# Kernel tuning notes

Measured on AMD Instinct MI355X. Metric: run time of the kernel, lower is better.

## Reference

```python
import jax, jax.numpy as jnp
from jax import lax
import numpy as np

N, C, H, W = 8, 32, 64, 64
KS, NB = 7, 6            # kernel_size, num_bases
TB = (KS // 2) * NB      # total_bases = 18
BC = TB * NB             # bc_dim = 108
INTER = max(64, BC // 2) # 64
OUT = 64
PAD = KS // 2
EPS = 1e-5


def conv3x3(x, w, b):
    # x: (N,Cin,H,W), w: (Cout,Cin,3,3)
    y = lax.conv_general_dilated(x, w, (1, 1), [(1, 1), (1, 1)],
                                 dimension_numbers=('NCHW', 'OIHW', 'NCHW'))
    return y + b[None, :, None, None]


def batchnorm(x, g, b):
    # training-mode BN: batch stats over (N,H,W)
    mu = jnp.mean(x, axis=(0, 2, 3), keepdims=True)
    var = jnp.var(x, axis=(0, 2, 3), keepdims=True)
    return (x - mu) * lax.rsqrt(var + EPS) * g[None, :, None, None] + b[None, :, None, None]


def setup_inputs() -> dict:
    key = jax.random.key(0)
    ks = jax.random.split(key, 12)
    s = 0.05
    # random bases as in get_random_bases: (TB, KS*KS), zero-mean-ish rows
    f = jax.random.normal(ks[0], (TB, KS * KS), dtype=jnp.float32)
    bases = f - jnp.mean(f, axis=1, keepdims=True) / jnp.std(f, axis=1, keepdims=True)
    return {
        'x': jax.random.normal(ks[1], (N, C, H, W), dtype=jnp.float32),
        'conv1_w': jax.random.normal(ks[2], (INTER, C, 3, 3), dtype=jnp.float32) * s,
        'conv1_b': jax.random.normal(ks[3], (INTER,), dtype=jnp.float32) * s,
        'bn1_g': jnp.ones((INTER,), jnp.float32),
        'bn1_b': jnp.zeros((INTER,), jnp.float32),
        'conv2_w': jax.random.normal(ks[4], (BC, INTER, 3, 3), dtype=jnp.float32) * s,
        'conv2_b': jax.random.normal(ks[5], (BC,), dtype=jnp.float32) * s,
        'bn2_g': jnp.ones((BC,), jnp.float32),
        'bn2_b': jnp.zeros((BC,), jnp.float32),
        'bases': bases,
        'out_w': jax.random.normal(ks[6], (OUT, C * NB), dtype=jnp.float32) * s,
        'out_b': jax.random.normal(ks[7], (OUT,), dtype=jnp.float32) * s,
    }


def reference(x, conv1_w, conv1_b, bn1_g, bn1_b, conv2_w, conv2_b,
              bn2_g, bn2_b, bases, out_w, out_b):
    # bases_net: conv3x3 -> BN -> tanh -> conv3x3 -> BN -> tanh
    h = jnp.tanh(batchnorm(conv3x3(x, conv1_w, conv1_b), bn1_g, bn1_b))
    coef = jnp.tanh(batchnorm(conv3x3(h, conv2_w, conv2_b), bn2_g, bn2_b))
    # (N, BC, H, W) -> (N, NB, TB, H, W) -> (N, H, W, NB, TB)
    coef = coef.reshape(N, NB, TB, H, W).transpose(0, 3, 4, 1, 2)
    # atoms: (coef[...,None] * bases).sum(-2).transpose(-1,-2) => (N,H,W,KS^2,NB)
    atoms = jnp.einsum('nhwmt,tk->nhwkm', coef, bases)
    # unfold: channel-major (C, ks, ks) flattened, matching F.unfold
    patches = lax.conv_general_dilated_patches(
        x, (KS, KS), (1, 1), [(PAD, PAD), (PAD, PAD)],
        dimension_numbers=('NCHW', 'OIHW', 'NCHW'))  # (N, C*KS*KS, H, W)
    patches = patches.reshape(N, C, KS * KS, H, W)
    # per-pixel contraction over ks^2: (N,H,W,C,NB)
    bases_out = jnp.einsum('nckhw,nhwkm->nhwcm', patches, atoms)
    bases_out = bases_out.reshape(N, H, W, C * NB)
    out = jnp.einsum('nhwd,od->nohw', bases_out, out_w) + out_b[None, :, None, None]
    return out
```

## Files before the change

### kernel.cpp

```cpp
#include <hip/hip_runtime.h>
#include <hip/hip_bf16.h>

#define N_ 8
#define C_ 32
#define H_ 64
#define W_ 64
#define HW_ (H_*W_)
#define NHW_ (N_*HW_)
#define INTER_ 64
#define BC_ 108
#define KS_ 7
#define K2_ (KS_*KS_)
#define NB_ 6
#define TB_ 18
#define OUT_ 64
#define DDIM_ (C_*NB_)
#define P2CH_ 288

typedef __attribute__((ext_vector_type(8))) short short8;
typedef __attribute__((ext_vector_type(4))) float f32x4;
typedef __attribute__((ext_vector_type(2))) float f32x2;

__device__ __forceinline__ unsigned short f2bf(float f) {
    union { float f; unsigned u; } v; v.f = f;
    unsigned r = v.u + 0x7fffu + ((v.u >> 16) & 1u);
    return (unsigned short)(r >> 16);
}
__device__ __forceinline__ float bf2f(unsigned short h) {
    return __uint_as_float((unsigned int)h << 16);
}

__device__ __forceinline__ short8 frag4(const unsigned int* p) {
    union { unsigned int u[4]; short8 s; } v;
    v.u[0] = p[0]; v.u[1] = p[1]; v.u[2] = p[2]; v.u[3] = p[3];
    return v.s;
}

__inline__ __device__ float wave_reduce_sum(float v) {
    #pragma unroll
    for (int off = 32; off > 0; off >>= 1) v += __shfl_down(v, off);
    return v;
}

template<int TP0, int NTP>
__device__ __forceinline__ void pconv_pass(const float (*sx)[44],
                                           const float* __restrict__ bases,
                                           unsigned int* __restrict__ P2,
                                           int n, int c, int r0, int rb, int lane) {
    f32x2 av[NTP][4];
    #pragma unroll
    for (int tp = 0; tp < NTP; tp++)
        #pragma unroll
        for (int rr = 0; rr < 4; rr++) av[tp][rr] = (f32x2){0.f, 0.f};

    #pragma unroll 1
    for (int kx = 0; kx < 7; kx++) {
        float rw[12];
        const float* sp = &sx[lane + kx][rb];
        #pragma unroll
        for (int qq = 0; qq < 3; qq++) {
            float4 r4 = *(const float4*)(sp + qq * 4);
            rw[qq * 4 + 0] = r4.x; rw[qq * 4 + 1] = r4.y;
            rw[qq * 4 + 2] = r4.z; rw[qq * 4 + 3] = r4.w;
        }
        #pragma unroll
        for (int tp = 0; tp < NTP; tp++) {
            #pragma unroll
            for (int ky = 0; ky < 7; ky++) {
                f32x2 w2;
                w2.x = bases[(2 * (TP0 + tp)) * K2_ + ky * 7 + kx];
                w2.y = bases[(2 * (TP0 + tp) + 1) * K2_ + ky * 7 + kx];
                #pragma unroll
                for (int rr = 0; rr < 4; rr++) {
                    float xv = rw[rr + ky];
                    f32x2 xv2 = (f32x2){xv, xv};
                    av[tp][rr] += xv2 * w2;
                }
            }
        }
    }

    #pragma unroll
    for (int tp = 0; tp < NTP; tp++)
        #pragma unroll
        for (int rr = 0; rr < 4; rr++) {
            int gr = r0 + rb + rr;
            unsigned int pk = (unsigned int)f2bf(av[tp][rr].x) |
                              ((unsigned int)f2bf(av[tp][rr].y) << 16);
            P2[(((size_t)n * P2CH_ + (TP0 + tp) * 32 + c) << 12) + (gr << 6) + lane] = pk;
        }
}

__global__ __launch_bounds__(256) void k_front(const float* __restrict__ x,
                                               const float* __restrict__ bases,
                                               const float* __restrict__ w1,
                                               const float* __restrict__ w2,
                                               const float* __restrict__ ow,
                                               unsigned short* __restrict__ xb,
                                               unsigned short* __restrict__ wb1,
                                               unsigned short* __restrict__ wb2,
                                               unsigned short* __restrict__ wbp,
                                               unsigned int* __restrict__ P2) {
    __shared__ __align__(16) char smem[70 * 44 * 4];
    int bid = blockIdx.x, t = threadIdx.x;

    if (bid < 1024) {
        float (*sx)[44] = (float(*)[44])smem;
        int rq = bid & 3;
        int c  = (bid >> 2) & 31;
        int n  = bid >> 7;
        int lane = t & 63, wv = t >> 6;
        int r0 = rq << 4;

        const float* xc = x + (((size_t)n * C_ + c) << 12);
        #pragma unroll
        for (int j = 0; j < 6; j++) {
            int p = wv + 4 * j;
            if (p < 22) {
                int grow = r0 - 3 + p;
                bool rowok = (grow >= 0 && grow < H_);
                int wx = lane - 3;
                float v = 0.f;
                if (rowok && wx >= 0) v = xc[(grow << 6) + wx];
                sx[lane][p] = v;
                if (lane < 6) {
                    int wx2 = 61 + lane;
                    float v2 = 0.f;
                    if (rowok && wx2 < W_) v2 = xc[(grow << 6) + wx2];
                    sx[64 + lane][p] = v2;
                }
            }
        }
        __syncthreads();

        int rb = wv * 4;
        pconv_pass<0, 5>(sx, bases, P2, n, c, r0, rb, lane);
        pconv_pass<5, 4>(sx, bases, P2, n, c, r0, rb, lane);
    } else {
        int pbid = bid - 1024;
        if (pbid < 512) {
            unsigned short* sT = (unsigned short*)smem;
            int n = pbid >> 6, hw0 = (pbid << 6) & 4095;
            for (int i = t; i < 2048; i += 256) {
                int c = i >> 6, px = i & 63;
                float v = x[(((size_t)n * C_ + c) << 12) + hw0 + px];
                sT[px * 36 + c] = f2bf(v);
            }
            __syncthreads();
            unsigned int* xd = (unsigned int*)xb;
            for (int i = t; i < 1024; i += 256) {
                int px = i >> 4, cw = i & 15;
                unsigned int lo = sT[px * 36 + cw * 2], hi = sT[px * 36 + cw * 2 + 1];
                xd[(((size_t)n << 12) + hw0 + px) * 16 + cw] = lo | (hi << 16);
            }
        } else if (pbid < 584) {
            int i = (pbid - 512) * 256 + t;
            int ci = i & 31, co = (i >> 5) & 63, s = i >> 11;
            wb1[i] = f2bf(w1[((co << 5) + ci) * 9 + s]);
        } else if (pbid < 872) {
            int i = (pbid - 584) * 256 + t;
            int ci = i & 63, co = (i >> 6) & 127, s = i >> 13;
            unsigned short v = 0;
            if (co < BC_) v = f2bf(w2[((co << 6) + ci) * 9 + s]);
            wb2[i] = v;
        } else {
            int i = (pbid - 872) * 256 + t;
            if (i < OUT_ * DDIM_) {
                float v = ow[i];
                unsigned short hi = f2bf(v);
                wbp[i] = hi;
                wbp[OUT_ * DDIM_ + i] = f2bf(v - bf2f(hi));
            }
        }
    }
}

template<int CIN, int COG, int ROWS, int WPAD, int NCOQ>
__global__ __launch_bounds__(256) void k_conv3(const unsigned short* __restrict__ xb,
                                               const unsigned short* __restrict__ wb,
                                               const float* __restrict__ bias,
                                               float* __restrict__ y,
                                               int COUT_real) {
    constexpr int CPAD = CIN + 8;
    constexpr int NSLC = (ROWS + 2) * 66;
    constexpr int MT = COG / 16;
    constexpr int NTW = ROWS;
    constexpr int KSTEPS = CIN / 32;
    __shared__ unsigned short sx[NSLC * CPAD];
    __shared__ unsigned short sw[9 * COG * CPAD];

    int bid = blockIdx.x;
    int coq = bid % NCOQ;
    int rp = (bid / NCOQ) % (H_ / ROWS);
    int n = bid / (NCOQ * (H_ / ROWS));
    int h0 = rp * ROWS;
    int co0 = coq * COG;
    int t = threadIdx.x;
    int lane = t & 63, wv = t >> 6;
    int q = lane >> 4, n15 = lane & 15;

    {
        const unsigned int* xg = (const unsigned int*)xb + (size_t)n * HW_ * (CIN / 2);
        unsigned int* sxd = (unsigned int*)sx;
        constexpr int DW = CIN / 2;
        constexpr int DWPT = DW / 8;
        int part = t & 7;
        for (int sl = (t >> 3); sl < NSLC; sl += 32) {
            int r = sl / 66, col = sl % 66;
            int hh = h0 - 1 + r, ww = col - 1;
            unsigned int v[DWPT];
            #pragma unroll
            for (int i = 0; i < DWPT; i++) v[i] = 0;
            if (hh >= 0 && hh < H_ && ww >= 0 && ww < W_) {
                const unsigned int* gp = xg + (size_t)(hh * W_ + ww) * DW + part * DWPT;
                #pragma unroll
                for (int i = 0; i < DWPT; i++) v[i] = gp[i];
            }
            unsigned int* d = sxd + sl * (CPAD / 2) + part * DWPT;
            #pragma unroll
            for (int i = 0; i < DWPT; i++) d[i] = v[i];
        }
    }
    {
        const unsigned int* wg = (const unsigned int*)wb;
        unsigned int* swd = (unsigned int*)sw;
        constexpr int TOT = 9 * COG * (CIN / 2);
        for (int e = t; e < TOT; e += 256) {
            int s_co = e / (CIN / 2), cw = e % (CIN / 2);
            int s = s_co / COG, co = s_co % COG;
            swd[s_co * (CPAD / 2) + cw] = wg[((size_t)s * WPAD + co0 + co) * (CIN / 2) + cw];
        }
    }
    __syncthreads();

    f32x4 acc[NTW][MT];
    #pragma unroll
    for (int a = 0; a < NTW; a++)
        #pragma unroll
        for (int m = 0; m < MT; m++) acc[a][m] = (f32x4){0.f, 0.f, 0.f, 0.f};

    #pragma unroll
    for (int s = 0; s < 9; s++) {
        int dy = s / 3, dx = s % 3;
        #pragma unroll
        for (int kc = 0; kc < KSTEPS; kc++) {
            int ci0 = kc * 32;
            short8 bfr[NTW];
            #pragma unroll
            for (int ntl = 0; ntl < NTW; ntl++) {
                int nt = wv * NTW + ntl;
                int r_out = nt >> 2, col0 = (nt & 3) * 16;
                bfr[ntl] = *(const short8*)(sx + ((r_out + dy) * 66 + col0 + n15 + dx) * CPAD + ci0 + q * 8);
            }
            #pragma unroll
            for (int mt = 0; mt < MT; mt++) {
                short8 afr = *(const short8*)(sw + ((s * COG) + mt * 16 + n15) * CPAD + ci0 + q * 8);
                #pragma unroll
                for (int ntl = 0; ntl < NTW; ntl++)
                    acc[ntl][mt] = __builtin_amdgcn_mfma_f32_16x16x32_bf16(afr, bfr[ntl], acc[ntl][mt], 0, 0, 0);
            }
        }
    }

    #pragma unroll
    for (int ntl = 0; ntl < NTW; ntl++) {
        int nt = wv * NTW + ntl;
        int h = h0 + (nt >> 2), wcol = (nt & 3) * 16 + n15;
        #pragma unroll
        for (int mt = 0; mt < MT; mt++) {
            #pragma unroll
            for (int reg = 0; reg < 4; reg++) {
                int co = co0 + mt * 16 + q * 4 + reg;
                if (co < COUT_real)
                    y[(((size_t)n * COUT_real + co) << 12) + h * W_ + wcol] = acc[ntl][mt][reg] + bias[co];
            }
        }
    }
}

__global__ __launch_bounds__(256) void k_bnpart(const float* __restrict__ y,
                                                float2* __restrict__ part, int Cout) {
    int bid = blockIdx.x;
    int c = bid >> 3, n = bid & 7;
    int t = threadIdx.x;
    const float* p = y + (((size_t)n * Cout + c) << 12) + t * 16;
    float s = 0.f, s2 = 0.f;
    #pragma unroll
    for (int j = 0; j < 4; j++) {
        float4 v = *(const float4*)(p + j * 4);
        s += v.x + v.y + v.z + v.w;
        s2 += v.x * v.x + v.y * v.y + v.z * v.z + v.w * v.w;
    }
    s = wave_reduce_sum(s);
    s2 = wave_reduce_sum(s2);
    __shared__ float sm[8];
    int wid = t >> 6, lane = t & 63;
    if (lane == 0) { sm[wid] = s; sm[4 + wid] = s2; }
    __syncthreads();
    if (t == 0) {
        float2 r;
        r.x = sm[0] + sm[1] + sm[2] + sm[3];
        r.y = sm[4] + sm[5] + sm[6] + sm[7];
        part[c * 8 + n] = r;
    }
}

__global__ __launch_bounds__(256) void k_bntr(const float* __restrict__ y1,
                                              const float2* __restrict__ part,
                                              const float* __restrict__ g,
                                              const float* __restrict__ bb,
                                              unsigned short* __restrict__ y1b) {
    __shared__ unsigned short sT[64 * 68];
    __shared__ float scs[INTER_], shs[INTER_];
    int bid = blockIdx.x, t = threadIdx.x;
    int n = bid >> 6, hw0 = (bid << 6) & 4095;
    if (t < INTER_) {
        float s = 0.f, s2 = 0.f;
        #pragma unroll
        for (int j = 0; j < 8; j++) { float2 p = part[t * 8 + j]; s += p.x; s2 += p.y; }
        float mu = s / (float)NHW_, var = s2 / (float)NHW_ - mu * mu;
        float sc = g[t] * rsqrtf(var + 1e-5f);
        scs[t] = sc; shs[t] = bb[t] - mu * sc;
    }
    __syncthreads();
    for (int i = t; i < 4096; i += 256) {
        int c = i >> 6, px = i & 63;
        float v = y1[(((size_t)n * INTER_ + c) << 12) + hw0 + px];
        sT[px * 68 + c] = f2bf(tanhf(v * scs[c] + shs[c]));
    }
    __syncthreads();
    unsigned int* yd = (unsigned int*)y1b;
    for (int i = t; i < 2048; i += 256) {
        int px = i >> 5, cw = i & 31;
        unsigned int lo = sT[px * 68 + cw * 2], hi = sT[px * 68 + cw * 2 + 1];
        yd[(((size_t)n << 12) + hw0 + px) * 32 + cw] = lo | (hi << 16);
    }
}

#define YPAD_ 97
__global__ __launch_bounds__(256) void k_ytail(const float* __restrict__ y2,
                                               const float2* __restrict__ part,
                                               const float* __restrict__ g,
                                               const float* __restrict__ bb,
                                               const unsigned int* __restrict__ P2,
                                               const unsigned short* __restrict__ wbp,
                                               const float* __restrict__ out_b,
                                               float* __restrict__ out) {
    __shared__ float scs[BC_], shs[BC_];
    __shared__ float cfs[BC_][32];
    __shared__ unsigned int sYh[32 * YPAD_];
    __shared__ unsigned int sYl[32 * YPAD_];

    int bid = blockIdx.x;
    int n = bid >> 7, px0 = (bid & 127) << 5;
    int t = threadIdx.x;

    int px = t & 31, cg = t >> 5;
    unsigned int u[4][9];
    {
        const unsigned int* Pb = P2 + (((size_t)n * P2CH_) << 12) + px0 + px;
        #pragma unroll
        for (int cc = 0; cc < 4; cc++) {
            int c = cg * 4 + cc;
            #pragma unroll
            for (int tp = 0; tp < 9; tp++)
                u[cc][tp] = Pb[(size_t)(tp * 32 + c) << 12];
        }
    }

    if (t < BC_) {
        float s = 0.f, s2 = 0.f;
        #pragma unroll
        for (int j = 0; j < 8; j++) { float2 p = part[t * 8 + j]; s += p.x; s2 += p.y; }
        float mu = s / (float)NHW_, var = s2 / (float)NHW_ - mu * mu;
        float sc = g[t] * rsqrtf(var + 1e-5f);
        scs[t] = sc; shs[t] = bb[t] - mu * sc;
    }
    __syncthreads();

    for (int i = t; i < BC_ * 32; i += 256) {
        int ch = i >> 5, pxx = i & 31;
        float v = y2[(((size_t)n * BC_ + ch) << 12) + px0 + pxx];
        cfs[ch][pxx] = tanhf(v * scs[ch] + shs[ch]);
    }
    __syncthreads();

    {
        f32x2 pv2[2][TB_];
        #pragma unroll
        for (int j = 0; j < 2; j++)
            #pragma unroll
            for (int tp = 0; tp < 9; tp++) {
                pv2[j][2 * tp].x     = __uint_as_float(u[2 * j][tp] << 16);
                pv2[j][2 * tp].y     = __uint_as_float(u[2 * j + 1][tp] << 16);
                pv2[j][2 * tp + 1].x = __uint_as_float(u[2 * j][tp] & 0xffff0000u);
                pv2[j][2 * tp + 1].y = __uint_as_float(u[2 * j + 1][tp] & 0xffff0000u);
            }
        f32x2 ym2[2][NB_];
        #pragma unroll
        for (int j = 0; j < 2; j++)
            #pragma unroll
            for (int m = 0; m < NB_; m++) ym2[j][m] = (f32x2){0.f, 0.f};
        #pragma unroll
        for (int m = 0; m < NB_; m++)
            #pragma unroll
            for (int tt = 0; tt < TB_; tt++) {
                float cfv = cfs[m * TB_ + tt][px];
                f32x2 c2 = (f32x2){cfv, cfv};
                ym2[0][m] += c2 * pv2[0][tt];
                ym2[1][m] += c2 * pv2[1][tt];
            }
        #pragma unroll
        for (int j = 0; j < 2; j++) {
            #pragma unroll
            for (int half = 0; half < 2; half++) {
                int c = cg * 4 + 2 * j + half;
                #pragma unroll
                for (int jj = 0; jj < 3; jj++) {
                    float y0 = half ? ym2[j][2 * jj].y     : ym2[j][2 * jj].x;
                    float y1v = half ? ym2[j][2 * jj + 1].y : ym2[j][2 * jj + 1].x;
                    unsigned short h0 = f2bf(y0);
                    unsigned short h1 = f2bf(y1v);
                    unsigned short l0 = f2bf(y0 - bf2f(h0));
                    unsigned short l1 = f2bf(y1v - bf2f(h1));
                    sYh[px * YPAD_ + c * 3 + jj] = (unsigned int)h0 | ((unsigned int)h1 << 16);
                    sYl[px * YPAD_ + c * 3 + jj] = (unsigned int)l0 | ((unsigned int)l1 << 16);
                }
            }
        }
    }
    __syncthreads();

    int lane = t & 63, wv = t >> 6;
    int q = lane >> 4, n15 = lane & 15;
    f32x4 acc[2];
    acc[0] = (f32x4){0.f, 0.f, 0.f, 0.f};
    acc[1] = (f32x4){0.f, 0.f, 0.f, 0.f};
    #pragma unroll
    for (int ks = 0; ks < 6; ks++) {
        short8 ah = *(const short8*)(wbp + (wv * 16 + n15) * DDIM_ + ks * 32 + q * 8);
        short8 al = *(const short8*)(wbp + OUT_ * DDIM_ + (wv * 16 + n15) * DDIM_ + ks * 32 + q * 8);
        #pragma unroll
        for (int nt = 0; nt < 2; nt++) {
            short8 bh = frag4(sYh + (nt * 16 + n15) * YPAD_ + ks * 16 + q * 4);
            short8 bl = frag4(sYl + (nt * 16 + n15) * YPAD_ + ks * 16 + q * 4);
            acc[nt] = __builtin_amdgcn_mfma_f32_16x16x32_bf16(ah, bh, acc[nt], 0, 0, 0);
            acc[nt] = __builtin_amdgcn_mfma_f32_16x16x32_bf16(ah, bl, acc[nt], 0, 0, 0);
            acc[nt] = __builtin_amdgcn_mfma_f32_16x16x32_bf16(al, bh, acc[nt], 0, 0, 0);
        }
    }
    #pragma unroll
    for (int nt = 0; nt < 2; nt++)
        #pragma unroll
        for (int reg = 0; reg < 4; reg++) {
            int o = wv * 16 + q * 4 + reg;
            out[(((size_t)n * OUT_ + o) << 12) + px0 + nt * 16 + n15] = acc[nt][reg] + out_b[o];
        }
}

extern "C" void kernel_launch(void* const* d_in, const int* in_sizes, int n_in,
                              void* d_out, int out_size, void* d_ws, size_t ws_size,
                              hipStream_t stream) {
    const float* x       = (const float*)d_in[0];
    const float* conv1_w = (const float*)d_in[1];
    const float* conv1_b = (const float*)d_in[2];
    const float* bn1_g   = (const float*)d_in[3];
    const float* bn1_b   = (const float*)d_in[4];
    const float* conv2_w = (const float*)d_in[5];
    const float* conv2_b = (const float*)d_in[6];
    const float* bn2_g   = (const float*)d_in[7];
    const float* bn2_b   = (const float*)d_in[8];
    const float* bases   = (const float*)d_in[9];
    const float* out_w   = (const float*)d_in[10];
    const float* out_b   = (const float*)d_in[11];
    float* out = (float*)d_out;

    float* y1  = (float*)d_ws;
    float* y2  = y1 + (size_t)N_ * INTER_ * HW_;
    unsigned int* P2 = (unsigned int*)(y2 + (size_t)N_ * BC_ * HW_);
    unsigned short* xb  = (unsigned short*)(P2 + (size_t)N_ * P2CH_ * HW_);
    unsigned short* y1b = xb + (size_t)NHW_ * C_;
    unsigned short* wb1 = y1b + (size_t)NHW_ * INTER_;
    unsigned short* wb2 = wb1 + 9 * 64 * 32;
    unsigned short* wbp = wb2 + 9 * 128 * 64;
    float2* part1 = (float2*)(wbp + 2 * OUT_ * DDIM_);
    float2* part2 = part1 + INTER_ * 8;

    k_front<<<1944, 256, 0, stream>>>(x, bases, conv1_w, conv2_w, out_w,
                                      xb, wb1, wb2, wbp, P2);

    k_conv3<C_, 64, 1, 64, 1><<<N_ * 64, 256, 0, stream>>>(
        xb, wb1, conv1_b, y1, INTER_);
    k_bnpart<<<INTER_ * 8, 256, 0, stream>>>(y1, part1, INTER_);
    k_bntr<<<512, 256, 0, stream>>>(y1, part1, bn1_g, bn1_b, y1b);

    k_conv3<INTER_, 16, 2, 128, 7><<<N_ * 32 * 7, 256, 0, stream>>>(
        y1b, wb2, conv2_b, y2, BC_);
    k_bnpart<<<BC_ * 8, 256, 0, stream>>>(y2, part2, BC_);

    k_ytail<<<1024, 256, 0, stream>>>(y2, (const float2*)part2, bn2_g, bn2_b,
                                      P2, wbp, out_b, out);
}
```

Before: 178.2 us.

## Fuse fp32-to-bf16 conversion into conv1 and merge BN1 stats into front kernel

Conv1 now reads fp32 x and fp32 weights directly, converting to bf16 while staging into shared memory. This removes the separate x transpose/convert pass and the weight prepack. The pixel-conv pass, BN1 partial statistics, and conv2/out weight packing are merged into one mid kernel launched after conv1, which drops one launch. In exchange, conv1 does strided per-channel global reads and every block repeats the weight conversion.

New measurement: 178.4 us. About the same (+0.1%).

```diff
diff --git a/kernel.cpp b/kernel.cpp
--- a/kernel.cpp
+++ b/kernel.cpp
@@ -91,16 +91,92 @@
         }
 }
 
-__global__ __launch_bounds__(256) void k_front(const float* __restrict__ x,
-                                               const float* __restrict__ bases,
-                                               const float* __restrict__ w1,
-                                               const float* __restrict__ w2,
-                                               const float* __restrict__ ow,
-                                               unsigned short* __restrict__ xb,
-                                               unsigned short* __restrict__ wb1,
-                                               unsigned short* __restrict__ wb2,
-                                               unsigned short* __restrict__ wbp,
-                                               unsigned int* __restrict__ P2) {
+__global__ __launch_bounds__(256) void k_conv1raw(const float* __restrict__ x,
+                                                  const float* __restrict__ w1,
+                                                  const float* __restrict__ bias,
+                                                  float* __restrict__ y) {
+    constexpr int CPAD = 40;
+    constexpr int NSLC = 3 * 66;
+    __shared__ unsigned short sx[NSLC * CPAD];
+    __shared__ unsigned short sw[9 * 64 * CPAD];
+
+    int bid = blockIdx.x;
+    int h0 = bid & 63;
+    int n = bid >> 6;
+    int t = threadIdx.x;
+    int lane = t & 63, wv = t >> 6;
+    int q = lane >> 4, n15 = lane & 15;
+
+    {
+        int part = t & 7;
+        for (int sl = (t >> 3); sl < NSLC; sl += 32) {
+            int r = sl / 66, col = sl % 66;
+            int hh = h0 - 1 + r, ww = col - 1;
+            unsigned int d0 = 0, d1 = 0;
+            if (hh >= 0 && hh < H_ && ww >= 0 && ww < W_) {
+                const float* xp = x + ((size_t)n * C_ + part * 4) * HW_ + hh * W_ + ww;
+                unsigned short b0 = f2bf(xp[0]);
+                unsigned short b1 = f2bf(xp[HW_]);
+                unsigned short b2 = f2bf(xp[2 * HW_]);
+                unsigned short b3 = f2bf(xp[3 * HW_]);
+                d0 = (unsigned int)b0 | ((unsigned int)b1 << 16);
+                d1 = (unsigned int)b2 | ((unsigned int)b3 << 16);
+            }
+            unsigned int* d = (unsigned int*)sx + sl * (CPAD / 2) + part * 2;
+            d[0] = d0; d[1] = d1;
+        }
+    }
+    {
+        #pragma unroll 2
+        for (int f = t * 8; f < t * 8 + 8; f++) {
+            int co = f >> 5, ci = f & 31;
+            const float* wp = w1 + (size_t)f * 9;
+            #pragma unroll
+            for (int s = 0; s < 9; s++)
+                sw[(s * 64 + co) * CPAD + ci] = f2bf(wp[s]);
+        }
+    }
+    __syncthreads();
+
+    f32x4 acc[4];
+    #pragma unroll
+    for (int m = 0; m < 4; m++) acc[m] = (f32x4){0.f, 0.f, 0.f, 0.f};
+
+    #pragma unroll
+    for (int s = 0; s < 9; s++) {
+        int dy = s / 3, dx = s % 3;
+        int nt = wv;
+        int col0 = (nt & 3) * 16;
+        short8 bfr = *(const short8*)(sx + (dy * 66 + col0 + n15 + dx) * CPAD + q * 8);
+        #pragma unroll
+        for (int mt = 0; mt < 4; mt++) {
+            short8 afr = *(const short8*)(sw + ((s * 64) + mt * 16 + n15) * CPAD + q * 8);
+            acc[mt] = __builtin_amdgcn_mfma_f32_16x16x32_bf16(afr, bfr, acc[mt], 0, 0, 0);
+        }
+    }
+
+    {
+        int wcol = (wv & 3) * 16 + n15;
+        #pragma unroll
+        for (int mt = 0; mt < 4; mt++) {
+            #pragma unroll
+            for (int reg = 0; reg < 4; reg++) {
+                int co = mt * 16 + q * 4 + reg;
+                y[(((size_t)n * INTER_ + co) << 12) + h0 * W_ + wcol] = acc[mt][reg] + bias[co];
+            }
+        }
+    }
+}
+
+__global__ __launch_bounds__(256) void k_mid(const float* __restrict__ x,
+                                             const float* __restrict__ bases,
+                                             const float* __restrict__ y1,
+                                             const float* __restrict__ w2,
+                                             const float* __restrict__ ow,
+                                             unsigned int* __restrict__ P2,
+                                             float2* __restrict__ part1,
+                                             unsigned short* __restrict__ wb2,
+                                             unsigned short* __restrict__ wbp) {
     __shared__ __align__(16) char smem[70 * 44 * 4];
     int bid = blockIdx.x, t = threadIdx.x;
 
@@ -136,64 +212,61 @@
         int rb = wv * 4;
         pconv_pass<0, 5>(sx, bases, P2, n, c, r0, rb, lane);
         pconv_pass<5, 4>(sx, bases, P2, n, c, r0, rb, lane);
+    } else if (bid < 1536) {
+        int pb = bid - 1024;
+        int c = pb >> 3, n = pb & 7;
+        const float* p = y1 + (((size_t)n * INTER_ + c) << 12) + t * 16;
+        float s = 0.f, s2 = 0.f;
+        #pragma unroll
+        for (int j = 0; j < 4; j++) {
+            float4 v = *(const float4*)(p + j * 4);
+            s += v.x + v.y + v.z + v.w;
+            s2 += v.x * v.x + v.y * v.y + v.z * v.z + v.w * v.w;
+        }
+        s = wave_reduce_sum(s);
+        s2 = wave_reduce_sum(s2);
+        float* sm = (float*)smem;
+        int wid = t >> 6, lane = t & 63;
+        if (lane == 0) { sm[wid] = s; sm[4 + wid] = s2; }
+        __syncthreads();
+        if (t == 0) {
+            float2 r;
+            r.x = sm[0] + sm[1] + sm[2] + sm[3];
+            r.y = sm[4] + sm[5] + sm[6] + sm[7];
+            part1[c * 8 + n] = r;
+        }
+    } else if (bid < 1824) {
+        int i = (bid - 1536) * 256 + t;
+        int ci = i & 63, co = (i >> 6) & 127, s = i >> 13;
+        unsigned short v = 0;
+        if (co < BC_) v = f2bf(w2[((co << 6) + ci) * 9 + s]);
+        wb2[i] = v;
     } else {
-        int pbid = bid - 1024;
-        if (pbid < 512) {
-            unsigned short* sT = (unsigned short*)smem;
-            int n = pbid >> 6, hw0 = (pbid << 6) & 4095;
-            for (int i = t; i < 2048; i += 256) {
-                int c = i >> 6, px = i & 63;
-                float v = x[(((size_t)n * C_ + c) << 12) + hw0 + px];
-                sT[px * 36 + c] = f2bf(v);
-            }
-            __syncthreads();
-            unsigned int* xd = (unsigned int*)xb;
-            for (int i = t; i < 1024; i += 256) {
-                int px = i >> 4, cw = i & 15;
-                unsigned int lo = sT[px * 36 + cw * 2], hi = sT[px * 36 + cw * 2 + 1];
-                xd[(((size_t)n << 12) + hw0 + px) * 16 + cw] = lo | (hi << 16);
-            }
-        } else if (pbid < 584) {
-            int i = (pbid - 512) * 256 + t;
-            int ci = i & 31, co = (i >> 5) & 63, s = i >> 11;
-            wb1[i] = f2bf(w1[((co << 5) + ci) * 9 + s]);
-        } else if (pbid < 872) {
-            int i = (pbid - 584) * 256 + t;
-            int ci = i & 63, co = (i >> 6) & 127, s = i >> 13;
-            unsigned short v = 0;
-            if (co < BC_) v = f2bf(w2[((co << 6) + ci) * 9 + s]);
-            wb2[i] = v;
-        } else {
-            int i = (pbid - 872) * 256 + t;
-            if (i < OUT_ * DDIM_) {
-                float v = ow[i];
-                unsigned short hi = f2bf(v);
-                wbp[i] = hi;
-                wbp[OUT_ * DDIM_ + i] = f2bf(v - bf2f(hi));
-            }
-        }
-    }
-}
-
-template<int CIN, int COG, int ROWS, int WPAD, int NCOQ>
-__global__ __launch_bounds__(256) void k_conv3(const unsigned short* __restrict__ xb,
+        int i = (bid - 1824) * 256 + t;
+        if (i < OUT_ * DDIM_) {
+            float v = ow[i];
+            unsigned short hi = f2bf(v);
+            wbp[i] = hi;
+            wbp[OUT_ * DDIM_ + i] = f2bf(v - bf2f(hi));
+        }
+    }
+}
+
+__global__ __launch_bounds__(256) void k_conv2(const unsigned short* __restrict__ xb,
                                                const unsigned short* __restrict__ wb,
                                                const float* __restrict__ bias,
-                                               float* __restrict__ y,
-                                               int COUT_real) {
+                                               float* __restrict__ y) {
+    constexpr int CIN = 64, COG = 16, WPAD = 128, NCOQ = 7;
     constexpr int CPAD = CIN + 8;
-    constexpr int NSLC = (ROWS + 2) * 66;
-    constexpr int MT = COG / 16;
-    constexpr int NTW = ROWS;
-    constexpr int KSTEPS = CIN / 32;
+    constexpr int NSLC = 4 * 66;
     __shared__ unsigned short sx[NSLC * CPAD];
     __shared__ unsigned short sw[9 * COG * CPAD];
 
     int bid = blockIdx.x;
     int coq = bid % NCOQ;
-    int rp = (bid / NCOQ) % (H_ / ROWS);
-    int n = bid / (NCOQ * (H_ / ROWS));
-    int h0 = rp * ROWS;
+    int rp = (bid / NCOQ) % 32;
+    int n = bid / (NCOQ * 32);
+    int h0 = rp * 2;
     int co0 = coq * COG;
     int t = threadIdx.x;
     int lane = t & 63, wv = t >> 6;
@@ -202,30 +275,27 @@
     {
         const unsigned int* xg = (const unsigned int*)xb + (size_t)n * HW_ * (CIN / 2);
         unsigned int* sxd = (unsigned int*)sx;
-        constexpr int DW = CIN / 2;
-        constexpr int DWPT = DW / 8;
         int part = t & 7;
         for (int sl = (t >> 3); sl < NSLC; sl += 32) {
             int r = sl / 66, col = sl % 66;
             int hh = h0 - 1 + r, ww = col - 1;
-            unsigned int v[DWPT];
-            #pragma unroll
-            for (int i = 0; i < DWPT; i++) v[i] = 0;
+            unsigned int v[4];
+            #pragma unroll
+            for (int i = 0; i < 4; i++) v[i] = 0;
             if (hh >= 0 && hh < H_ && ww >= 0 && ww < W_) {
-                const unsigned int* gp = xg + (size_t)(hh * W_ + ww) * DW + part * DWPT;
+                const unsigned int* gp = xg + (size_t)(hh * W_ + ww) * 32 + part * 4;
                 #pragma unroll
-                for (int i = 0; i < DWPT; i++) v[i] = gp[i];
-            }
-            unsigned int* d = sxd + sl * (CPAD / 2) + part * DWPT;
-            #pragma unroll
-            for (int i = 0; i < DWPT; i++) d[i] = v[i];
+                for (int i = 0; i < 4; i++) v[i] = gp[i];
+            }
+            unsigned int* d = sxd + sl * (CPAD / 2) + part * 4;
+            #pragma unroll
+            for (int i = 0; i < 4; i++) d[i] = v[i];
         }
     }
     {
         const unsigned int* wg = (const unsigned int*)wb;
         unsigned int* swd = (unsigned int*)sw;
-        constexpr int TOT = 9 * COG * (CIN / 2);
-        for (int e = t; e < TOT; e += 256) {
+        for (int e = t; e < 9 * COG * (CIN / 2); e += 256) {
             int s_co = e / (CIN / 2), cw = e % (CIN / 2);
             int s = s_co / COG, co = s_co % COG;
             swd[s_co * (CPAD / 2) + cw] = wg[((size_t)s * WPAD + co0 + co) * (CIN / 2) + cw];
@@ -233,47 +303,38 @@
     }
     __syncthreads();
 
-    f32x4 acc[NTW][MT];
-    #pragma unroll
-    for (int a = 0; a < NTW; a++)
-        #pragma unroll
-        for (int m = 0; m < MT; m++) acc[a][m] = (f32x4){0.f, 0.f, 0.f, 0.f};
+    f32x4 acc[2];
+    acc[0] = (f32x4){0.f, 0.f, 0.f, 0.f};
+    acc[1] = (f32x4){0.f, 0.f, 0.f, 0.f};
 
     #pragma unroll
     for (int s = 0; s < 9; s++) {
         int dy = s / 3, dx = s % 3;
         #pragma unroll
-        for (int kc = 0; kc < KSTEPS; kc++) {
+        for (int kc = 0; kc < 2; kc++) {
             int ci0 = kc * 32;
-            short8 bfr[NTW];
-            #pragma unroll
-            for (int ntl = 0; ntl < NTW; ntl++) {
-                int nt = wv * NTW + ntl;
+            short8 bfr[2];
+            #pragma unroll
+            for (int ntl = 0; ntl < 2; ntl++) {
+                int nt = wv * 2 + ntl;
                 int r_out = nt >> 2, col0 = (nt & 3) * 16;
                 bfr[ntl] = *(const short8*)(sx + ((r_out + dy) * 66 + col0 + n15 + dx) * CPAD + ci0 + q * 8);
             }
-            #pragma unroll
-            for (int mt = 0; mt < MT; mt++) {
-                short8 afr = *(const short8*)(sw + ((s * COG) + mt * 16 + n15) * CPAD + ci0 + q * 8);
-                #pragma unroll
-                for (int ntl = 0; ntl < NTW; ntl++)
-                    acc[ntl][mt] = __builtin_amdgcn_mfma_f32_16x16x32_bf16(afr, bfr[ntl], acc[ntl][mt], 0, 0, 0);
-            }
-        }
-    }
-
-    #pragma unroll
-    for (int ntl = 0; ntl < NTW; ntl++) {
-        int nt = wv * NTW + ntl;
+            short8 afr = *(const short8*)(sw + (s * COG + n15) * CPAD + ci0 + q * 8);
+            acc[0] = __builtin_amdgcn_mfma_f32_16x16x32_bf16(afr, bfr[0], acc[0], 0, 0, 0);
+            acc[1] = __builtin_amdgcn_mfma_f32_16x16x32_bf16(afr, bfr[1], acc[1], 0, 0, 0);
+        }
+    }
+
+    #pragma unroll
+    for (int ntl = 0; ntl < 2; ntl++) {
+        int nt = wv * 2 + ntl;
         int h = h0 + (nt >> 2), wcol = (nt & 3) * 16 + n15;
         #pragma unroll
-        for (int mt = 0; mt < MT; mt++) {
-            #pragma unroll
-            for (int reg = 0; reg < 4; reg++) {
-                int co = co0 + mt * 16 + q * 4 + reg;
-                if (co < COUT_real)
-                    y[(((size_t)n * COUT_real + co) << 12) + h * W_ + wcol] = acc[ntl][mt][reg] + bias[co];
-            }
+        for (int reg = 0; reg < 4; reg++) {
+            int co = co0 + q * 4 + reg;
+            if (co < BC_)
+                y[(((size_t)n * BC_ + co) << 12) + h * W_ + wcol] = acc[ntl][reg] + bias[co];
         }
     }
 }
@@ -478,24 +539,20 @@
     float* y1  = (float*)d_ws;
     float* y2  = y1 + (size_t)N_ * INTER_ * HW_;
     unsigned int* P2 = (unsigned int*)(y2 + (size_t)N_ * BC_ * HW_);
-    unsigned short* xb  = (unsigned short*)(P2 + (size_t)N_ * P2CH_ * HW_);
-    unsigned short* y1b = xb + (size_t)NHW_ * C_;
-    unsigned short* wb1 = y1b + (size_t)NHW_ * INTER_;
-    unsigned short* wb2 = wb1 + 9 * 64 * 32;
+    unsigned short* y1b = (unsigned short*)(P2 + (size_t)N_ * P2CH_ * HW_);
+    unsigned short* wb2 = y1b + (size_t)NHW_ * INTER_;
     unsigned short* wbp = wb2 + 9 * 128 * 64;
     float2* part1 = (float2*)(wbp + 2 * OUT_ * DDIM_);
     float2* part2 = part1 + INTER_ * 8;
 
-    k_front<<<1944, 256, 0, stream>>>(x, bases, conv1_w, conv2_w, out_w,
-                                      xb, wb1, wb2, wbp, P2);
-
-    k_conv3<C_, 64, 1, 64, 1><<<N_ * 64, 256, 0, stream>>>(
-        xb, wb1, conv1_b, y1, INTER_);
-    k_bnpart<<<INTER_ * 8, 256, 0, stream>>>(y1, part1, INTER_);
+    k_conv1raw<<<N_ * 64, 256, 0, stream>>>(x, conv1_w, conv1_b, y1);
+
+    k_mid<<<1872, 256, 0, stream>>>(x, bases, y1, conv2_w, out_w,
+                                    P2, part1, wb2, wbp);
+
     k_bntr<<<512, 256, 0, stream>>>(y1, part1, bn1_g, bn1_b, y1b);
 
-    k_conv3<INTER_, 16, 2, 128, 7><<<N_ * 32 * 7, 256, 0, stream>>>(
-        y1b, wb2, conv2_b, y2, BC_);
+    k_conv2<<<N_ * 32 * 7, 256, 0, stream>>>(y1b, wb2, conv2_b, y2);
     k_bnpart<<<BC_ * 8, 256, 0, stream>>>(y2, part2, BC_);
 
     k_ytail<<<1024, 256, 0, stream>>>(y2, (const float2*)part2, bn2_g, bn2_b,
```
